# Optimization experiments

Measured on AMD Instinct MI355X. Metric: run time of the kernel, lower is better.

Reference implementation:

```python
import jax, jax.numpy as jnp
import numpy as np
import math

D_MODEL = 512
NUM_NEURONS = 512
LUT_SIZE = 4096
TWO_PI = 2.0 * math.pi


def setup_inputs() -> dict:
    key = jax.random.key(0)
    ks = jax.random.split(key, 4)
    x = jax.random.normal(ks[0], (4, 256, D_MODEL), dtype=jnp.float32)
    W = jax.random.normal(ks[1], (NUM_NEURONS, D_MODEL), dtype=jnp.float32) * 0.02
    B = jnp.zeros((NUM_NEURONS, D_MODEL), dtype=jnp.float32)
    attn_cos = jnp.ones((NUM_NEURONS, D_MODEL), dtype=jnp.float32)
    attn_sin = jnp.ones((NUM_NEURONS, D_MODEL), dtype=jnp.float32)
    # xavier_uniform with gain=0.5 for Linear(num_neurons -> d_model)
    limit = 0.5 * math.sqrt(6.0 / (NUM_NEURONS + D_MODEL))
    proj_cos_w = jax.random.uniform(ks[2], (D_MODEL, NUM_NEURONS), minval=-limit, maxval=limit, dtype=jnp.float32)
    proj_sin_w = jax.random.uniform(ks[3], (D_MODEL, NUM_NEURONS), minval=-limit, maxval=limit, dtype=jnp.float32)
    # global sin/cos LUT sampled uniformly over one period
    phase = jnp.arange(LUT_SIZE, dtype=jnp.float32) * (TWO_PI / LUT_SIZE)
    sin_table = jnp.sin(phase)
    cos_table = jnp.cos(phase)
    return {"x": x, "W": W, "B": B, "attn_cos": attn_cos, "attn_sin": attn_sin,
            "proj_cos_w": proj_cos_w, "proj_sin_w": proj_sin_w,
            "sin_table": sin_table, "cos_table": cos_table}


def reference(x, W, B, attn_cos, attn_sin, proj_cos_w, proj_sin_w, sin_table, cos_table):
    # theta: [b, s, num_neurons, d_model]
    wavelength = 1.0 + jnp.abs(W)
    theta = x[..., None, :] / wavelength + B
    # LUT lookup: nearest-index into a table sampled over [0, 2pi)
    res = sin_table.shape[0]
    idx = jnp.mod(jnp.round(theta * (res / TWO_PI)).astype(jnp.int32), res)
    sin_theta = sin_table[idx]
    cos_theta = cos_table[idx]
    # weighted reduction over d_model -> [b, s, num_neurons]
    cos_sum = jnp.sum(cos_theta * attn_cos, axis=-1)
    sin_sum = jnp.sum(sin_theta * attn_sin, axis=-1)
    # dual projections back to d_model: [b, s, d_model]
    out = jnp.einsum('bsn,dn->bsd', cos_sum, proj_cos_w) + jnp.einsum('bsn,dn->bsd', sin_sum, proj_sin_w)
    return jax.nn.silu(out)
```

## Files before the change

### kernel.cpp

```cpp
#include <hip/hip_runtime.h>
#include <math.h>

#define DM 512
#define NN 512
#define SCALE 651.8986469044033f
#define MAGIC 12582912.0f

__device__ __forceinline__ unsigned bf16rne(float f) {
    unsigned u = __float_as_uint(f);
    return (u + 0x7fffu + ((u >> 16) & 1u)) >> 16;
}

__global__ __launch_bounds__(256) void kprep(
    const float* __restrict__ W, const float* __restrict__ B,
    const float* __restrict__ AC, const float* __restrict__ AS,
    const float* __restrict__ PC, const float* __restrict__ PS,
    float4* __restrict__ packAB, unsigned* __restrict__ projTb)
{
    __shared__ float4 tile4[64][65];
    const int tid = threadIdx.x;
    const int tx = tid & 63, ty = tid >> 6;
    const int mode = blockIdx.x >> 6;
    const int tl = blockIdx.x & 63;
    const int r0 = (tl >> 3) * 64;
    const int c0 = (tl & 7) * 64;

    if (mode == 0) {
#pragma unroll
        for (int p = 0; p < 16; ++p) {
            int r = p * 4 + ty;
            int src = (r0 + r) * DM + c0 + tx;
            float w = W[src], b = B[src];
            tile4[r][tx] = make_float4(SCALE / (1.0f + fabsf(w)),
                                       fmaf(b, SCALE, MAGIC), AC[src], AS[src]);
        }
        __syncthreads();
#pragma unroll
        for (int p = 0; p < 16; ++p) {
            int c = p * 4 + ty;
            packAB[(c0 + c) * NN + r0 + tx] = tile4[tx][c];
        }
    } else {
        float2* t2 = (float2*)tile4;
#pragma unroll
        for (int p = 0; p < 16; ++p) {
            int r = p * 4 + ty;
            int src = (r0 + r) * NN + c0 + tx;
            t2[r * 65 + tx] = make_float2(PC[src], PS[src]);
        }
        __syncthreads();
#pragma unroll
        for (int p = 0; p < 16; ++p) {
            int c = p * 4 + ty;
            float2 v = t2[tx * 65 + c];
            projTb[(c0 + c) * DM + r0 + tx] = bf16rne(v.x) | (bf16rne(v.y) << 16);
        }
    }
}

__global__ __launch_bounds__(512, 8) void kmain(
    const float* __restrict__ x,
    const float* __restrict__ sinT, const float* __restrict__ cosT,
    const float4* __restrict__ packAB,
    float2* __restrict__ pairs)
{
    __shared__ unsigned lut[4096];
    __shared__ float xT[512][8];
    __shared__ float2 accL[8][64];

    const int tid  = threadIdx.x;
    const int bid  = blockIdx.x;
    const int tile = bid >> 3, ng = bid & 7;
    const int lane = tid & 63;
    const int wv   = __builtin_amdgcn_readfirstlane(tid >> 6);
    const int t0   = tile * 8;

#pragma unroll
    for (int j = 0; j < 8; ++j) {
        int k = tid + j * 512;
        lut[k] = bf16rne(sinT[k]) | (bf16rne(cosT[k]) << 16);
    }
    {
        const int tt = tid & 7, dr = tid >> 3;
#pragma unroll
        for (int c = 0; c < 8; ++c) {
            int d = c * 64 + dr;
            xT[d][tt] = x[(t0 + tt) * DM + d];
        }
    }
    ((float2*)accL)[tid] = make_float2(0.f, 0.f);
    __syncthreads();

    float accC[8], accS[8];
#pragma unroll
    for (int t = 0; t < 8; ++t) { accC[t] = 0.f; accS[t] = 0.f; }

    const float4* pAB = packAB + (wv * 64) * NN + ng * 64 + lane;

#pragma unroll 2
    for (int i = 0; i < 64; ++i) {
        float4 a = pAB[i * NN];
        const float4* xr = (const float4*)&xT[wv * 64 + i][0];
        float4 xq0 = xr[0], xq1 = xr[1];
        float xv[8] = {xq0.x, xq0.y, xq0.z, xq0.w, xq1.x, xq1.y, xq1.z, xq1.w};
#pragma unroll
        for (int t = 0; t < 8; ++t) {
            float f  = fmaf(xv[t], a.x, a.y);
            unsigned u = lut[__float_as_uint(f) & 4095u];
            accC[t] = fmaf(__uint_as_float(u & 0xffff0000u), a.z, accC[t]);
            accS[t] = fmaf(__uint_as_float(u << 16),         a.w, accS[t]);
        }
    }

#pragma unroll
    for (int t = 0; t < 8; ++t) {
        atomicAdd(&accL[t][lane].x, accC[t]);
        atomicAdd(&accL[t][lane].y, accS[t]);
    }
    __syncthreads();
    {
        int t = tid >> 6, n = tid & 63;
        float2 v = accL[t][n];
        pairs[(t0 + t) * NN + ng * 64 + n] = v;
    }
}

__global__ __launch_bounds__(512) void kproj(
    const float2* __restrict__ pairs, const uint4* __restrict__ projTb,
    float* __restrict__ out)
{
    __shared__ float2 pl[8][NN];
    __shared__ float4 part[512];
    const int bid  = blockIdx.x;
    const int tile = bid >> 2, dg = bid & 3;
    const int tid  = threadIdx.x;
    const int dslot = tid & 31;
    const int tg   = (tid >> 5) & 7;
    const int nh   = tid >> 8;
    const int t0   = tile * 8;

    {
        const float4* src = (const float4*)(pairs + t0 * NN);
        float4* dst = (float4*)pl;
#pragma unroll
        for (int k = 0; k < 4; ++k) dst[tid + k * 512] = src[tid + k * 512];
    }
    __syncthreads();

    const int gslot = dg * 32 + dslot;
    const uint4* pp = projTb + nh * (256 * 128) + gslot;
    const float2* pt = &pl[tg][nh * 256];
    float4 acc = make_float4(0.f, 0.f, 0.f, 0.f);
#pragma unroll 4
    for (int n = 0; n < 256; ++n) {
        uint4 q = pp[n * 128];
        float2 cs = pt[n];
        acc.x = fmaf(__uint_as_float(q.x << 16), cs.x, acc.x);
        acc.x = fmaf(__uint_as_float(q.x & 0xffff0000u), cs.y, acc.x);
        acc.y = fmaf(__uint_as_float(q.y << 16), cs.x, acc.y);
        acc.y = fmaf(__uint_as_float(q.y & 0xffff0000u), cs.y, acc.y);
        acc.z = fmaf(__uint_as_float(q.z << 16), cs.x, acc.z);
        acc.z = fmaf(__uint_as_float(q.z & 0xffff0000u), cs.y, acc.z);
        acc.w = fmaf(__uint_as_float(q.w << 16), cs.x, acc.w);
        acc.w = fmaf(__uint_as_float(q.w & 0xffff0000u), cs.y, acc.w);
    }
    part[tid] = acc;
    __syncthreads();
    if (tid < 256) {
        float4 a = part[tid], b = part[tid + 256];
        float4 s = make_float4(a.x + b.x, a.y + b.y, a.z + b.z, a.w + b.w);
        float4 o;
        o.x = s.x / (1.f + __expf(-s.x));
        o.y = s.y / (1.f + __expf(-s.y));
        o.z = s.z / (1.f + __expf(-s.z));
        o.w = s.w / (1.f + __expf(-s.w));
        *(float4*)(out + (t0 + tg) * DM + gslot * 4) = o;
    }
}

extern "C" void kernel_launch(void* const* d_in, const int* in_sizes, int n_in,
                              void* d_out, int out_size, void* d_ws, size_t ws_size,
                              hipStream_t stream)
{
    const float* x    = (const float*)d_in[0];
    const float* W    = (const float*)d_in[1];
    const float* B    = (const float*)d_in[2];
    const float* AC   = (const float*)d_in[3];
    const float* AS   = (const float*)d_in[4];
    const float* PC   = (const float*)d_in[5];
    const float* PS   = (const float*)d_in[6];
    const float* sinT = (const float*)d_in[7];
    const float* cosT = (const float*)d_in[8];
    float* out = (float*)d_out;

    char* ws = (char*)d_ws;
    float4*   packAB = (float4*)ws;
    unsigned* projTb = (unsigned*)(ws + (4u << 20));
    float2*   pairs  = (float2*)(ws + (6u << 20));

    kprep<<<128, 256, 0, stream>>>(W, B, AC, AS, PC, PS, packAB, projTb);
    kmain<<<1024, 512, 0, stream>>>(x, sinT, cosT, packAB, pairs);
    kproj<<<512, 512, 0, stream>>>(pairs, (const uint4*)projTb, out);
}
```

Measured before the change: 198.2 us.

## Split phase work between LUT and hardware sin/cos; use bf16 MFMA for projection

In the main kernel, five of the eight waves per block still use the shared-memory LUT for sin/cos. The other three waves compute the phase with fract and call the hardware sin/cos instructions, with the prep kernel writing the matching 1/(2π) scaling for those d_model columns. This spreads the work between LDS random lookups and the transcendental units. The reduced cos/sin sums are now stored as interleaved bf16 pairs. The projection kernel is rewritten as a 16x16x32 bf16 MFMA GEMM over the interleaved K=1024 dimension with SiLU fused into the store, replacing the scalar FMA loop. The catch is that the hardware sin/cos no longer reproduces the reference's nearest-index table rounding, and rounding the sums to bf16 adds precision error.

After: 179.1 us. -9.6%, faster.

```diff
diff --git a/kernel.cpp b/kernel.cpp
--- a/kernel.cpp
+++ b/kernel.cpp
@@ -5,6 +5,12 @@
 #define NN 512
 #define SCALE 651.8986469044033f
 #define MAGIC 12582912.0f
+#define INV2PI 0.15915494309189535f
+#define NLW 5
+#define DSPLIT (NLW * 64)
+
+typedef __attribute__((ext_vector_type(8))) short short8v;
+typedef __attribute__((ext_vector_type(4))) float f32x4;
 
 __device__ __forceinline__ unsigned bf16rne(float f) {
     unsigned u = __float_as_uint(f);
@@ -26,13 +32,19 @@
     const int c0 = (tl & 7) * 64;
 
     if (mode == 0) {
+        const int d = c0 + tx;
 #pragma unroll
         for (int p = 0; p < 16; ++p) {
             int r = p * 4 + ty;
-            int src = (r0 + r) * DM + c0 + tx;
+            int src = (r0 + r) * DM + d;
             float w = W[src], b = B[src];
-            tile4[r][tx] = make_float4(SCALE / (1.0f + fabsf(w)),
-                                       fmaf(b, SCALE, MAGIC), AC[src], AS[src]);
+            float iw = 1.0f + fabsf(w);
+            float4 v;
+            if (d < DSPLIT)
+                v = make_float4(SCALE / iw, fmaf(b, SCALE, MAGIC), AC[src], AS[src]);
+            else
+                v = make_float4(INV2PI / iw, b * INV2PI, AC[src], AS[src]);
+            tile4[r][tx] = v;
         }
         __syncthreads();
 #pragma unroll
@@ -41,19 +53,11 @@
             packAB[(c0 + c) * NN + r0 + tx] = tile4[tx][c];
         }
     } else {
-        float2* t2 = (float2*)tile4;
 #pragma unroll
         for (int p = 0; p < 16; ++p) {
             int r = p * 4 + ty;
             int src = (r0 + r) * NN + c0 + tx;
-            t2[r * 65 + tx] = make_float2(PC[src], PS[src]);
-        }
-        __syncthreads();
-#pragma unroll
-        for (int p = 0; p < 16; ++p) {
-            int c = p * 4 + ty;
-            float2 v = t2[tx * 65 + c];
-            projTb[(c0 + c) * DM + r0 + tx] = bf16rne(v.x) | (bf16rne(v.y) << 16);
+            projTb[src] = bf16rne(PC[src]) | (bf16rne(PS[src]) << 16);
         }
     }
 }
@@ -62,7 +66,7 @@
     const float* __restrict__ x,
     const float* __restrict__ sinT, const float* __restrict__ cosT,
     const float4* __restrict__ packAB,
-    float2* __restrict__ pairs)
+    unsigned* __restrict__ pairsb)
 {
     __shared__ unsigned lut[4096];
     __shared__ float xT[512][8];
@@ -97,18 +101,34 @@
 
     const float4* pAB = packAB + (wv * 64) * NN + ng * 64 + lane;
 
+    if (wv < NLW) {
 #pragma unroll 2
-    for (int i = 0; i < 64; ++i) {
-        float4 a = pAB[i * NN];
-        const float4* xr = (const float4*)&xT[wv * 64 + i][0];
-        float4 xq0 = xr[0], xq1 = xr[1];
-        float xv[8] = {xq0.x, xq0.y, xq0.z, xq0.w, xq1.x, xq1.y, xq1.z, xq1.w};
-#pragma unroll
-        for (int t = 0; t < 8; ++t) {
-            float f  = fmaf(xv[t], a.x, a.y);
-            unsigned u = lut[__float_as_uint(f) & 4095u];
-            accC[t] = fmaf(__uint_as_float(u & 0xffff0000u), a.z, accC[t]);
-            accS[t] = fmaf(__uint_as_float(u << 16),         a.w, accS[t]);
+        for (int i = 0; i < 64; ++i) {
+            float4 a = pAB[i * NN];
+            const float4* xr = (const float4*)&xT[wv * 64 + i][0];
+            float4 xq0 = xr[0], xq1 = xr[1];
+            float xv[8] = {xq0.x, xq0.y, xq0.z, xq0.w, xq1.x, xq1.y, xq1.z, xq1.w};
+#pragma unroll
+            for (int t = 0; t < 8; ++t) {
+                float f  = fmaf(xv[t], a.x, a.y);
+                unsigned u = lut[__float_as_uint(f) & 4095u];
+                accC[t] = fmaf(__uint_as_float(u & 0xffff0000u), a.z, accC[t]);
+                accS[t] = fmaf(__uint_as_float(u << 16),         a.w, accS[t]);
+            }
+        }
+    } else {
+#pragma unroll 2
+        for (int i = 0; i < 64; ++i) {
+            float4 a = pAB[i * NN];
+            const float4* xr = (const float4*)&xT[wv * 64 + i][0];
+            float4 xq0 = xr[0], xq1 = xr[1];
+            float xv[8] = {xq0.x, xq0.y, xq0.z, xq0.w, xq1.x, xq1.y, xq1.z, xq1.w};
+#pragma unroll
+            for (int t = 0; t < 8; ++t) {
+                float ph = __builtin_amdgcn_fractf(fmaf(xv[t], a.x, a.y));
+                accC[t] = fmaf(__builtin_amdgcn_cosf(ph), a.z, accC[t]);
+                accS[t] = fmaf(__builtin_amdgcn_sinf(ph), a.w, accS[t]);
+            }
         }
     }
 
@@ -121,60 +141,41 @@
     {
         int t = tid >> 6, n = tid & 63;
         float2 v = accL[t][n];
-        pairs[(t0 + t) * NN + ng * 64 + n] = v;
-    }
-}
-
-__global__ __launch_bounds__(512) void kproj(
-    const float2* __restrict__ pairs, const uint4* __restrict__ projTb,
+        pairsb[(t0 + t) * NN + ng * 64 + n] = bf16rne(v.x) | (bf16rne(v.y) << 16);
+    }
+}
+
+__global__ __launch_bounds__(256) void kproj(
+    const unsigned* __restrict__ pairsb, const unsigned* __restrict__ projTb,
     float* __restrict__ out)
 {
-    __shared__ float2 pl[8][NN];
-    __shared__ float4 part[512];
-    const int bid  = blockIdx.x;
-    const int tile = bid >> 2, dg = bid & 3;
     const int tid  = threadIdx.x;
-    const int dslot = tid & 31;
-    const int tg   = (tid >> 5) & 7;
-    const int nh   = tid >> 8;
-    const int t0   = tile * 8;
-
-    {
-        const float4* src = (const float4*)(pairs + t0 * NN);
-        float4* dst = (float4*)pl;
-#pragma unroll
-        for (int k = 0; k < 4; ++k) dst[tid + k * 512] = src[tid + k * 512];
-    }
-    __syncthreads();
-
-    const int gslot = dg * 32 + dslot;
-    const uint4* pp = projTb + nh * (256 * 128) + gslot;
-    const float2* pt = &pl[tg][nh * 256];
-    float4 acc = make_float4(0.f, 0.f, 0.f, 0.f);
+    const int lane = tid & 63;
+    const int w    = tid >> 6;
+    const int tileIdx = blockIdx.x * 4 + w;
+    const int tt = tileIdx >> 5;
+    const int dt = tileIdx & 31;
+    const int r16 = lane & 15;
+    const int kg  = lane >> 4;
+
+    const short* Af = (const short*)pairsb;
+    const short* Bf = (const short*)projTb;
+    const short8v* pa = (const short8v*)(Af + (tt * 16 + r16) * 1024 + kg * 8);
+    const short8v* pb = (const short8v*)(Bf + (dt * 16 + r16) * 1024 + kg * 8);
+
+    f32x4 acc = {0.f, 0.f, 0.f, 0.f};
 #pragma unroll 4
-    for (int n = 0; n < 256; ++n) {
-        uint4 q = pp[n * 128];
-        float2 cs = pt[n];
-        acc.x = fmaf(__uint_as_float(q.x << 16), cs.x, acc.x);
-        acc.x = fmaf(__uint_as_float(q.x & 0xffff0000u), cs.y, acc.x);
-        acc.y = fmaf(__uint_as_float(q.y << 16), cs.x, acc.y);
-        acc.y = fmaf(__uint_as_float(q.y & 0xffff0000u), cs.y, acc.y);
-        acc.z = fmaf(__uint_as_float(q.z << 16), cs.x, acc.z);
-        acc.z = fmaf(__uint_as_float(q.z & 0xffff0000u), cs.y, acc.z);
-        acc.w = fmaf(__uint_as_float(q.w << 16), cs.x, acc.w);
-        acc.w = fmaf(__uint_as_float(q.w & 0xffff0000u), cs.y, acc.w);
-    }
-    part[tid] = acc;
-    __syncthreads();
-    if (tid < 256) {
-        float4 a = part[tid], b = part[tid + 256];
-        float4 s = make_float4(a.x + b.x, a.y + b.y, a.z + b.z, a.w + b.w);
-        float4 o;
-        o.x = s.x / (1.f + __expf(-s.x));
-        o.y = s.y / (1.f + __expf(-s.y));
-        o.z = s.z / (1.f + __expf(-s.z));
-        o.w = s.w / (1.f + __expf(-s.w));
-        *(float4*)(out + (t0 + tg) * DM + gslot * 4) = o;
+    for (int kk = 0; kk < 32; ++kk) {
+        short8v a = pa[kk * 4];
+        short8v b = pb[kk * 4];
+        acc = __builtin_amdgcn_mfma_f32_16x16x32_bf16(a, b, acc, 0, 0, 0);
+    }
+#pragma unroll
+    for (int r = 0; r < 4; ++r) {
+        int m = kg * 4 + r;
+        float s = acc[r];
+        float o = s / (1.f + __expf(-s));
+        out[(tt * 16 + m) * DM + dt * 16 + r16] = o;
     }
 }
 
@@ -196,9 +197,9 @@
     char* ws = (char*)d_ws;
     float4*   packAB = (float4*)ws;
     unsigned* projTb = (unsigned*)(ws + (4u << 20));
-    float2*   pairs  = (float2*)(ws + (6u << 20));
+    unsigned* pairsb = (unsigned*)(ws + (6u << 20));
 
     kprep<<<128, 256, 0, stream>>>(W, B, AC, AS, PC, PS, packAB, projTb);
-    kmain<<<1024, 512, 0, stream>>>(x, sinT, cosT, packAB, pairs);
-    kproj<<<512, 512, 0, stream>>>(pairs, (const uint4*)projTb, out);
-}
+    kmain<<<1024, 512, 0, stream>>>(x, sinT, cosT, packAB, pairsb);
+    kproj<<<512, 256, 0, stream>>>(pairsb, projTb, out);
+}
```
